# Kernel tuning notes

Hardware: AMD Instinct MI355X
Metric: run time of the kernel (lower is better)

## Reference

```python
import jax, jax.numpy as jnp
import numpy as np
from jax import lax

K = 3            # kernel_size
STRIDE = 2
PADDING = 1
OUT_PADDING = 1
DILATION = 1


def setup_inputs() -> dict:
    key = jax.random.key(0)
    x = jax.random.normal(key, (16, 64, 64, 64), dtype=jnp.float32)
    return {"x": x}


def _unfold_transpose2d(x):
    """im2col for transpose convolution via one-hot grouped conv-transpose.

    Matches torch.nn.functional.conv_transpose2d(x, W, stride, padding,
    output_padding, dilation, groups=C) with W[c, h*K+w, h, w] = 1 (one-hot),
    followed by reshape to [B, C*K*K, L].
    """
    B, C, H, W = x.shape
    KK = K * K
    # One-hot kernel: [KK, 1, K, K], tiled per input channel -> [C*KK, 1, K, K]
    eye = jnp.eye(KK, dtype=x.dtype).reshape(KK, 1, K, K)
    weight = jnp.tile(eye, (C, 1, 1, 1))
    # conv_transpose == conv with lhs dilation and spatially flipped kernel
    w_flip = weight[:, :, ::-1, ::-1]
    pad_lo = DILATION * (K - 1) - PADDING
    pad_hi = pad_lo + OUT_PADDING
    out = lax.conv_general_dilated(
        x,
        w_flip,
        window_strides=(1, 1),
        padding=[(pad_lo, pad_hi), (pad_lo, pad_hi)],
        lhs_dilation=(STRIDE, STRIDE),
        rhs_dilation=(DILATION, DILATION),
        dimension_numbers=("NCHW", "OIHW", "NCHW"),
        feature_group_count=C,
    )  # [B, C*KK, H_out, W_out]
    return out.reshape(B, C * KK, -1)


def reference(x):
    return _unfold_transpose2d(x)
```

## Files before the change

kernel.cpp:

```cpp
#include <hip/hip_runtime.h>


__global__ __launch_bounds__(256) void unfold_t2d_kernel(
    const float* __restrict__ x, float* __restrict__ out) {
    int lane = threadIdx.x & 63;
    int wid  = blockIdx.x * 4 + (threadIdx.x >> 6);
    int cc   = wid / 9;
    int j    = wid - cc * 9;
    int jh   = j / 3;
    int jw   = j - jh * 3;
    int p    = (1 - jw) & 1;
    int dlt  = (jw == 0) ? 1 : 0;
    int iwl  = lane + dlt;
    bool wv  = iwl < 64;

    const float* xc = x + cc * 4096;
    float2* ob = reinterpret_cast<float2*>(out + ((size_t)wid << 14)) + lane;

#pragma unroll 4
    for (int oh = 0; oh < 128; ++oh) {
        int rh = oh + 1 - jh;
        int ih = rh >> 1;
        bool hv = (rh >= 0) & ((rh & 1) == 0) & (ih < 64);
        float v = 0.f;
        if (hv & wv) v = xc[ih * 64 + iwl];
        float2 o;
        o.x = (p == 0) ? v : 0.f;
        o.y = (p == 1) ? v : 0.f;
        ob[(size_t)oh * 64] = o;
    }
}

extern "C" void kernel_launch(void* const* d_in, const int* in_sizes, int n_in,
                              void* d_out, int out_size, void* d_ws, size_t ws_size,
                              hipStream_t stream) {
    const float* x = (const float*)d_in[0];
    float* out = (float*)d_out;
    unfold_t2d_kernel<<<2304, 256, 0, stream>>>(x, out);
}
```

Measured before the change: 662.4 us.

## Stage each channel plane in LDS and emit all nine taps with float4 stores

Each block now loads one 64x64 input channel plane into shared memory with float4 loads, then writes half of the output rows for all nine kernel taps. The stores widen from float2 to float4. The aim is to read each input plane from global memory once per block instead of once per tap-warp, and to issue fewer, wider stores for this write-bound op. It adds about 16KB of LDS per block and a barrier, which may limit occupancy.

```diff
diff --git a/kernel.cpp b/kernel.cpp
--- a/kernel.cpp
+++ b/kernel.cpp
@@ -3,31 +3,48 @@
 
 __global__ __launch_bounds__(256) void unfold_t2d_kernel(
     const float* __restrict__ x, float* __restrict__ out) {
-    int lane = threadIdx.x & 63;
-    int wid  = blockIdx.x * 4 + (threadIdx.x >> 6);
-    int cc   = wid / 9;
-    int j    = wid - cc * 9;
-    int jh   = j / 3;
-    int jw   = j - jh * 3;
-    int p    = (1 - jw) & 1;
-    int dlt  = (jw == 0) ? 1 : 0;
-    int iwl  = lane + dlt;
-    bool wv  = iwl < 64;
+    __shared__ float lds[64 * 64 + 68];
+    int tid = threadIdx.x;
+    int bid = blockIdx.x;
+    int cc  = bid >> 1;
+    int h   = bid & 1;
 
-    const float* xc = x + cc * 4096;
-    float2* ob = reinterpret_cast<float2*>(out + ((size_t)wid << 14)) + lane;
+    const float4* xs = reinterpret_cast<const float4*>(x + cc * 4096);
+    float4* ls = reinterpret_cast<float4*>(lds);
+#pragma unroll
+    for (int i = 0; i < 4; ++i) ls[i * 256 + tid] = xs[i * 256 + tid];
+    __syncthreads();
 
-#pragma unroll 4
-    for (int oh = 0; oh < 128; ++oh) {
-        int rh = oh + 1 - jh;
-        int ih = rh >> 1;
-        bool hv = (rh >= 0) & ((rh & 1) == 0) & (ih < 64);
-        float v = 0.f;
-        if (hv & wv) v = xc[ih * 64 + iwl];
-        float2 o;
-        o.x = (p == 0) ? v : 0.f;
-        o.y = (p == 1) ? v : 0.f;
-        ob[(size_t)oh * 64] = o;
+    int fw = tid & 31;
+    int rb = tid >> 5;
+    float4* outb = reinterpret_cast<float4*>(out)
+                 + (size_t)cc * 9 * 4096 + h * 2048;
+
+#pragma unroll
+    for (int j = 0; j < 9; ++j) {
+        const int jh  = j / 3, jw = j % 3;
+        const int dlt = (jw == 0) ? 1 : 0;
+        const int p   = (1 - jw) & 1;
+        int  colw = 2 * fw + dlt;
+        bool edge = (jw == 0) && (fw == 31);
+        float4* oj = outb + j * 4096;
+#pragma unroll
+        for (int it = 0; it < 8; ++it) {
+            int oh = h * 64 + it * 8 + rb;
+            int rh = oh + 1 - jh;
+            int ih = rh >> 1;
+            bool hv = (rh >= 0) & ((rh & 1) == 0) & (ih < 64);
+            int ihc = hv ? ih : 0;
+            int base = ihc * 64 + colw;
+            float sx = lds[base];
+            float sy = lds[base + 1];
+            sx = hv ? sx : 0.f;
+            sy = (hv && !edge) ? sy : 0.f;
+            float4 o;
+            if (p == 0) { o.x = sx;  o.y = 0.f; o.z = sy;  o.w = 0.f; }
+            else        { o.x = 0.f; o.y = sx;  o.z = 0.f; o.w = sy;  }
+            oj[it * 256 + tid] = o;
+        }
     }
 }
 
@@ -36,5 +53,5 @@
                               hipStream_t stream) {
     const float* x = (const float*)d_in[0];
     float* out = (float*)d_out;
-    unfold_t2d_kernel<<<2304, 256, 0, stream>>>(x, out);
+    unfold_t2d_kernel<<<2048, 256, 0, stream>>>(x, out);
 }
```

New measurement: 601.3 us. -9.2%, faster.
